# Kernel tuning notes

Hardware: AMD Instinct MI355X
Metric: run time of the kernel (lower is better)

The kernel has to match this reference:

```python
import jax, jax.numpy as jnp
import numpy as np

MUL_VAL = 4.0

def _fake_quant(v, qmin, qmax):
    # per-tensor float scale from abs-max (brevitas Int8*PerTensorFloat style)
    s = jnp.max(jnp.abs(v)) / 127.0
    q = jnp.clip(jnp.round(v / s), qmin, qmax) * s
    return q

def setup_inputs() -> dict:
    key = jax.random.key(0)
    k1, k2, k3 = jax.random.split(key, 3)
    N, IN, OUT = 8192, 4096, 4096
    x = jax.random.normal(k1, (N, IN), dtype=jnp.float32)
    W = jax.random.normal(k2, (OUT, IN), dtype=jnp.float32) * 0.02
    b = jax.random.normal(k3, (OUT,), dtype=jnp.float32) * 0.01
    return {"x": x, "W": W, "b": b}

def reference(x, W, b):
    # Int8ActPerTensorFloat: signed 8-bit, non-narrow range [-128, 127]
    qx = _fake_quant(x, -128.0, 127.0)
    # Int8WeightPerTensorFloat: signed 8-bit, narrow range [-127, 127]
    qw = _fake_quant(W, -127.0, 127.0)
    y = jnp.einsum('ni,oi->no', qx, qw) + b
    return MUL_VAL * y
```

## Files before the change

### kernel.cpp

```cpp
#include <hip/hip_runtime.h>

typedef int int4v __attribute__((ext_vector_type(4)));
typedef int int16v __attribute__((ext_vector_type(16)));

#define BM 256
#define BN 256
#define BKB 128

__device__ __forceinline__ void async_copy16(const void* g, void* l) {
  __builtin_amdgcn_global_load_lds((const __attribute__((address_space(1))) void*)g,
                                   (__attribute__((address_space(3))) void*)l, 16, 0, 0);
}

__global__ __launch_bounds__(256) void absmax2_kernel(
    const float* __restrict__ x, size_t n4x,
    const float* __restrict__ w, size_t n4w,
    unsigned* __restrict__ out, int xb) {
  const float4* src;
  size_t n4;
  unsigned* dst;
  int bid, nb;
  if ((int)blockIdx.x < xb) {
    src = (const float4*)x; n4 = n4x; dst = out; bid = blockIdx.x; nb = xb;
  } else {
    src = (const float4*)w; n4 = n4w; dst = out + 1; bid = blockIdx.x - xb; nb = gridDim.x - xb;
  }
  size_t i = (size_t)bid * blockDim.x + threadIdx.x;
  size_t stride = (size_t)nb * blockDim.x;
  float m = 0.0f;
  for (; i < n4; i += stride) {
    float4 v = src[i];
    m = fmaxf(m, fmaxf(fmaxf(fabsf(v.x), fabsf(v.y)), fmaxf(fabsf(v.z), fabsf(v.w))));
  }
#pragma unroll
  for (int off = 32; off > 0; off >>= 1)
    m = fmaxf(m, __shfl_down(m, off, 64));
  __shared__ float red[4];
  int wave = threadIdx.x >> 6, lane = threadIdx.x & 63;
  if (lane == 0) red[wave] = m;
  __syncthreads();
  if (threadIdx.x == 0) {
    m = fmaxf(fmaxf(red[0], red[1]), fmaxf(red[2], red[3]));
    atomicMax(dst, __float_as_uint(m));
  }
}

__global__ __launch_bounds__(256) void quant2_kernel(
    const float* __restrict__ x, char* __restrict__ qx, size_t nx,
    const float* __restrict__ w, char* __restrict__ qw, size_t nw,
    const unsigned* __restrict__ amax, int xb) {
  const float* src;
  char* dst;
  size_t n;
  float r, lo;
  int bid, nb;
  if ((int)blockIdx.x < xb) {
    src = x; dst = qx; n = nx; r = 127.0f / __uint_as_float(amax[0]);
    lo = -128.0f; bid = blockIdx.x; nb = xb;
  } else {
    src = w; dst = qw; n = nw; r = 127.0f / __uint_as_float(amax[1]);
    lo = -127.0f; bid = blockIdx.x - xb; nb = gridDim.x - xb;
  }
  size_t i = ((size_t)bid * blockDim.x + threadIdx.x) * 8;
  size_t stride = (size_t)nb * blockDim.x * 8;
  for (; i < n; i += stride) {
    float4 v0 = *(const float4*)(src + i);
    float4 v1 = *(const float4*)(src + i + 4);
    float f[8] = {v0.x, v0.y, v0.z, v0.w, v1.x, v1.y, v1.z, v1.w};
    unsigned w0 = 0, w1 = 0;
#pragma unroll
    for (int j = 0; j < 4; ++j) {
      int q0 = (int)fminf(fmaxf(rintf(f[j] * r), lo), 127.0f);
      int q1 = (int)fminf(fmaxf(rintf(f[4 + j] * r), lo), 127.0f);
      w0 |= (unsigned)(q0 & 0xff) << (8 * j);
      w1 |= (unsigned)(q1 & 0xff) << (8 * j);
    }
    uint2 u; u.x = w0; u.y = w1;
    *(uint2*)(dst + i) = u;
  }
}


#define STAGE_ALL(buf_, t_) do {                                               \
    const char* ga_ = gA + (size_t)(t_) * BKB;                                 \
    const char* gb_ = gB + (size_t)(t_) * BKB;                                 \
    int r0_ = wave * 8;                                                        \
    async_copy16(ga_ + (size_t)(r0_      ) * K, &As[buf_][(r0_      ) * BKB]); \
    async_copy16(ga_ + (size_t)(r0_ +  64) * K, &As[buf_][(r0_ +  64) * BKB]); \
    async_copy16(ga_ + (size_t)(r0_ + 128) * K, &As[buf_][(r0_ + 128) * BKB]); \
    async_copy16(ga_ + (size_t)(r0_ + 192) * K, &As[buf_][(r0_ + 192) * BKB]); \
    async_copy16(gb_ + (size_t)(r0_      ) * K, &Bs[buf_][(r0_      ) * BKB]); \
    async_copy16(gb_ + (size_t)(r0_ +  64) * K, &Bs[buf_][(r0_ +  64) * BKB]); \
    async_copy16(gb_ + (size_t)(r0_ + 128) * K, &Bs[buf_][(r0_ + 128) * BKB]); \
    async_copy16(gb_ + (size_t)(r0_ + 192) * K, &Bs[buf_][(r0_ + 192) * BKB]); \
  } while (0)

#define VM0 asm volatile("s_waitcnt vmcnt(0)" ::: "memory")
#define BAR do { asm volatile("" ::: "memory");                                \
                 __builtin_amdgcn_s_barrier();                                 \
                 asm volatile("" ::: "memory"); } while (0)

#define MFMA32 __builtin_amdgcn_mfma_i32_32x32x32_i8

#define KSTEP(so_) do {                                                        \
    int4v a0_ = *(const int4v*)(Ab_ + 0 * 32 * BKB + (so_));                   \
    int4v a1_ = *(const int4v*)(Ab_ + 1 * 32 * BKB + (so_));                   \
    int4v a2_ = *(const int4v*)(Ab_ + 2 * 32 * BKB + (so_));                   \
    int4v a3_ = *(const int4v*)(Ab_ + 3 * 32 * BKB + (so_));                   \
    int4v b0_ = *(const int4v*)(Bb_ + 0 * 32 * BKB + (so_));                   \
    int4v b1_ = *(const int4v*)(Bb_ + 1 * 32 * BKB + (so_));                   \
    __builtin_amdgcn_s_setprio(1);                                             \
    acc[0][0] = MFMA32(a0_, b0_, acc[0][0], 0, 0, 0);                          \
    acc[0][1] = MFMA32(a0_, b1_, acc[0][1], 0, 0, 0);                          \
    acc[1][0] = MFMA32(a1_, b0_, acc[1][0], 0, 0, 0);                          \
    acc[1][1] = MFMA32(a1_, b1_, acc[1][1], 0, 0, 0);                          \
    acc[2][0] = MFMA32(a2_, b0_, acc[2][0], 0, 0, 0);                          \
    acc[2][1] = MFMA32(a2_, b1_, acc[2][1], 0, 0, 0);                          \
    acc[3][0] = MFMA32(a3_, b0_, acc[3][0], 0, 0, 0);                          \
    acc[3][1] = MFMA32(a3_, b1_, acc[3][1], 0, 0, 0);                          \
    __builtin_amdgcn_s_setprio(0);                                             \
  } while (0)

#define COMPUTE(bb_) do {                                                      \
    const char* Ab_ = &As[bb_][(wr * 128 + r32) * BKB];                        \
    const char* Bb_ = &Bs[bb_][(wc * 64 + r32) * BKB];                         \
    KSTEP(so0); KSTEP(so1); KSTEP(so2); KSTEP(so3);                            \
  } while (0)

__global__ __launch_bounds__(512, 2) void gemm_i8_kernel(
    const char* __restrict__ qx, const char* __restrict__ qw,
    const float* __restrict__ bias, const unsigned* __restrict__ amax,
    float* __restrict__ out, int M, int N, int K) {
  __shared__ __align__(16) char As[2][BM * BKB];
  __shared__ __align__(16) char Bs[2][BN * BKB];
  const int tid = threadIdx.x;
  const int wave = tid >> 6, lane = tid & 63;
  const int wr = wave >> 2, wc = wave & 3;

  int tilesM = M / BM, tilesN = N / BN;
  int T = tilesM * tilesN;
  int p = blockIdx.x;
  int tile;
  if ((T & 7) == 0) tile = (p & 7) * (T >> 3) + (p >> 3);
  else tile = p;
  int bm = (tile % tilesM) * BM;
  int bn = (tile / tilesM) * BN;

  const int grow = lane >> 3;
  const int gcol = ((lane & 7) ^ grow) * 16;
  const char* gA = qx + (size_t)(bm + grow) * K + gcol;
  const char* gB = qw + (size_t)(bn + grow) * K + gcol;

  const int r32 = lane & 31, hi = lane >> 5, l7 = lane & 7;
  const int so0 = ((0 + hi) ^ l7) * 16;
  const int so1 = ((2 + hi) ^ l7) * 16;
  const int so2 = ((4 + hi) ^ l7) * 16;
  const int so3 = ((6 + hi) ^ l7) * 16;

  const int NT = K >> 7;

  int16v acc[4][2] = {};

  STAGE_ALL(0, 0);
  VM0;
  BAR;

  int t = 0;
  for (; t < NT - 2; t += 2) {
    STAGE_ALL(1, t + 1);
    COMPUTE(0);
    VM0; BAR;
    STAGE_ALL(0, t + 2);
    COMPUTE(1);
    VM0; BAR;
  }
  STAGE_ALL(1, NT - 1);
  COMPUTE(0);
  VM0; BAR;
  COMPUTE(1);

  float fx = __uint_as_float(amax[0]) * (1.0f / 127.0f);
  float fw = __uint_as_float(amax[1]) * (1.0f / 127.0f);
  float scale = 4.0f * fx * fw;
  int col = lane & 31;
  int rbh = 4 * hi;
#pragma unroll
  for (int n = 0; n < 2; ++n) {
    int gn = bn + wc * 64 + n * 32 + col;
    float b4 = 4.0f * bias[gn];
#pragma unroll
    for (int m = 0; m < 4; ++m) {
      size_t rowb = (size_t)(bm + wr * 128 + m * 32 + rbh);
#pragma unroll
      for (int g = 0; g < 4; ++g)
#pragma unroll
        for (int rr = 0; rr < 4; ++rr)
          __builtin_nontemporal_store(
              scale * (float)acc[m][n][g * 4 + rr] + b4,
              out + (rowb + g * 8 + rr) * N + gn);
    }
  }
}

extern "C" void kernel_launch(void* const* d_in, const int* in_sizes, int n_in,
                              void* d_out, int out_size, void* d_ws, size_t ws_size,
                              hipStream_t stream) {
  const float* x = (const float*)d_in[0];
  const float* W = (const float*)d_in[1];
  const float* b = (const float*)d_in[2];
  float* out = (float*)d_out;

  int Nv = in_sizes[2];
  int K = in_sizes[1] / Nv;
  int M = in_sizes[0] / K;

  size_t nx = (size_t)M * K, nw = (size_t)Nv * K;
  unsigned* amax = (unsigned*)d_ws;
  char* qx = (char*)d_ws + 256;
  char* qw = qx + nx;

  hipMemsetAsync(d_ws, 0, 8, stream);
  absmax2_kernel<<<1536, 256, 0, stream>>>(x, nx / 4, W, nw / 4, amax, 1024);
  quant2_kernel<<<3072, 256, 0, stream>>>(x, qx, nx, W, qw, nw, amax, 2048);
  gemm_i8_kernel<<<(M / BM) * (Nv / BN), 512, 0, stream>>>(qx, qw, b, amax, out, M, Nv, K);
}
```

Measured before the change: 442.8 us.

## Interleave staging loads with per-kstep barriers in int8 GEMM main loop

Restructures the int8 GEMM main loop into four phases per K tile. Each phase reads its LDS fragments, issues part of the next tile's async global-to-LDS copies, and synchronizes with barriers around its MFMA block, so all waves in a block issue MFMAs in lockstep. Spreading the copies across phases is meant to smooth memory issue and overlap it with compute. The cost is two extra barriers per k-step, which risks added stalls.

```diff
diff --git a/kernel.cpp b/kernel.cpp
--- a/kernel.cpp
+++ b/kernel.cpp
@@ -81,14 +81,18 @@
 }
 
 
-#define STAGE_ALL(buf_, t_) do {                                               \
+#define STAGE_A4(buf_, t_) do {                                                \
     const char* ga_ = gA + (size_t)(t_) * BKB;                                 \
-    const char* gb_ = gB + (size_t)(t_) * BKB;                                 \
     int r0_ = wave * 8;                                                        \
     async_copy16(ga_ + (size_t)(r0_      ) * K, &As[buf_][(r0_      ) * BKB]); \
     async_copy16(ga_ + (size_t)(r0_ +  64) * K, &As[buf_][(r0_ +  64) * BKB]); \
     async_copy16(ga_ + (size_t)(r0_ + 128) * K, &As[buf_][(r0_ + 128) * BKB]); \
     async_copy16(ga_ + (size_t)(r0_ + 192) * K, &As[buf_][(r0_ + 192) * BKB]); \
+  } while (0)
+
+#define STAGE_B4(buf_, t_) do {                                                \
+    const char* gb_ = gB + (size_t)(t_) * BKB;                                 \
+    int r0_ = wave * 8;                                                        \
     async_copy16(gb_ + (size_t)(r0_      ) * K, &Bs[buf_][(r0_      ) * BKB]); \
     async_copy16(gb_ + (size_t)(r0_ +  64) * K, &Bs[buf_][(r0_ +  64) * BKB]); \
     async_copy16(gb_ + (size_t)(r0_ + 128) * K, &Bs[buf_][(r0_ + 128) * BKB]); \
@@ -96,19 +100,23 @@
   } while (0)
 
 #define VM0 asm volatile("s_waitcnt vmcnt(0)" ::: "memory")
-#define BAR do { asm volatile("" ::: "memory");                                \
-                 __builtin_amdgcn_s_barrier();                                 \
-                 asm volatile("" ::: "memory"); } while (0)
+#define VMN ((void)0)
+#define NOSTG ((void)0)
 
 #define MFMA32 __builtin_amdgcn_mfma_i32_32x32x32_i8
 
-#define KSTEP(so_) do {                                                        \
+#define PHASE(bb_, so_, STG, VMW) do {                                         \
+    asm volatile("" ::: "memory");                                             \
+    const char* Ab_ = &As[bb_][(wr * 128 + r32) * BKB];                        \
+    const char* Bb_ = &Bs[bb_][(wc * 64 + r32) * BKB];                         \
     int4v a0_ = *(const int4v*)(Ab_ + 0 * 32 * BKB + (so_));                   \
     int4v a1_ = *(const int4v*)(Ab_ + 1 * 32 * BKB + (so_));                   \
     int4v a2_ = *(const int4v*)(Ab_ + 2 * 32 * BKB + (so_));                   \
     int4v a3_ = *(const int4v*)(Ab_ + 3 * 32 * BKB + (so_));                   \
     int4v b0_ = *(const int4v*)(Bb_ + 0 * 32 * BKB + (so_));                   \
     int4v b1_ = *(const int4v*)(Bb_ + 1 * 32 * BKB + (so_));                   \
+    STG;                                                                       \
+    __builtin_amdgcn_s_barrier();                                              \
     __builtin_amdgcn_s_setprio(1);                                             \
     acc[0][0] = MFMA32(a0_, b0_, acc[0][0], 0, 0, 0);                          \
     acc[0][1] = MFMA32(a0_, b1_, acc[0][1], 0, 0, 0);                          \
@@ -119,12 +127,16 @@
     acc[3][0] = MFMA32(a3_, b0_, acc[3][0], 0, 0, 0);                          \
     acc[3][1] = MFMA32(a3_, b1_, acc[3][1], 0, 0, 0);                          \
     __builtin_amdgcn_s_setprio(0);                                             \
-  } while (0)
-
-#define COMPUTE(bb_) do {                                                      \
-    const char* Ab_ = &As[bb_][(wr * 128 + r32) * BKB];                        \
-    const char* Bb_ = &Bs[bb_][(wc * 64 + r32) * BKB];                         \
-    KSTEP(so0); KSTEP(so1); KSTEP(so2); KSTEP(so3);                            \
+    VMW;                                                                       \
+    asm volatile("" ::: "memory");                                             \
+    __builtin_amdgcn_s_barrier();                                              \
+  } while (0)
+
+#define TILE(bb_, STG0, STG1, VMW3) do {                                       \
+    PHASE(bb_, so0, STG0, VMN);                                                \
+    PHASE(bb_, so1, STG1, VMN);                                                \
+    PHASE(bb_, so2, NOSTG, VMN);                                               \
+    PHASE(bb_, so3, NOSTG, VMW3);                                              \
   } while (0)
 
 __global__ __launch_bounds__(512, 2) void gemm_i8_kernel(
@@ -161,23 +173,18 @@
 
   int16v acc[4][2] = {};
 
-  STAGE_ALL(0, 0);
+  STAGE_A4(0, 0);
+  STAGE_B4(0, 0);
   VM0;
-  BAR;
+  __builtin_amdgcn_s_barrier();
 
   int t = 0;
   for (; t < NT - 2; t += 2) {
-    STAGE_ALL(1, t + 1);
-    COMPUTE(0);
-    VM0; BAR;
-    STAGE_ALL(0, t + 2);
-    COMPUTE(1);
-    VM0; BAR;
-  }
-  STAGE_ALL(1, NT - 1);
-  COMPUTE(0);
-  VM0; BAR;
-  COMPUTE(1);
+    TILE(0, STAGE_A4(1, t + 1), STAGE_B4(1, t + 1), VM0);
+    TILE(1, STAGE_A4(0, t + 2), STAGE_B4(0, t + 2), VM0);
+  }
+  TILE(0, STAGE_A4(1, NT - 1), STAGE_B4(1, NT - 1), VM0);
+  TILE(1, NOSTG, NOSTG, VMN);
 
   float fx = __uint_as_float(amax[0]) * (1.0f / 127.0f);
   float fw = __uint_as_float(amax[1]) * (1.0f / 127.0f);
```

Result: no change. 443.5 us (+0.1%).
